# Kernel optimization log

Hardware: AMD Instinct MI355X
Metric: run time of the kernel (lower is better)

The kernel has to match this reference:

```python
import jax, jax.numpy as jnp
import numpy as np

NUM_HEADS = 16

def setup_inputs() -> dict:
    key = jax.random.key(0)
    ks = jax.random.split(key, 6)
    B, S, D = 2, 2048, 1024
    x = jax.random.normal(ks[0], (B, S, D), dtype=jnp.float32)
    s = 1.0 / np.sqrt(D)
    Wq = jax.random.normal(ks[1], (D, D), dtype=jnp.float32) * s
    Wk = jax.random.normal(ks[2], (D, D), dtype=jnp.float32) * s
    Wv = jax.random.normal(ks[3], (D, D), dtype=jnp.float32) * s
    Wff = jax.random.normal(ks[4], (D, D), dtype=jnp.float32) * s
    bff = jax.random.normal(ks[5], (D,), dtype=jnp.float32) * 0.01
    return {"x": x, "Wq": Wq, "Wk": Wk, "Wv": Wv, "Wff": Wff, "bff": bff}

def reference(x, Wq, Wk, Wv, Wff, bff):
    B, S, D = x.shape
    H = NUM_HEADS
    Dh = D // H
    # Q/K/V projections (bias-free Linears). Original scales Q by 1/sqrt(hidden_size).
    q = (x @ Wq.T) * (1.0 / jnp.sqrt(jnp.asarray(D, x.dtype)))
    k = x @ Wk.T
    v = x @ Wv.T
    q = q.reshape(B, S, H, Dh)
    k = k.reshape(B, S, H, Dh)
    v = v.reshape(B, S, H, Dh)
    # Blockwise online-softmax attention is mathematically identical to
    # full softmax attention over all keys (no causal mask in source).
    scores = jnp.einsum('bqhd,bkhd->bhqk', q, k)
    attn = jax.nn.softmax(scores, axis=-1)
    out = jnp.einsum('bhqk,bkhd->bqhd', attn, v).reshape(B, S, D)
    # Final feedforward Linear(hidden, hidden) with bias.
    return out @ Wff.T + bff
```

## Files before the change

kernel.cpp:

```cpp
#include <hip/hip_runtime.h>
#include <stdint.h>

typedef __attribute__((ext_vector_type(8))) short bf16x8;
typedef __attribute__((ext_vector_type(4))) float f32x4;

__device__ __forceinline__ uint16_t f2bf(float f) {
  union { float f; uint32_t u; } a; a.f = f;
  uint32_t u = a.u;
  u += 0x7FFFu + ((u >> 16) & 1u);
  return (uint16_t)(u >> 16);
}

__device__ __forceinline__ uint32_t pk_bf16(float a, float b) {
#if __has_builtin(__builtin_amdgcn_cvt_pk_bf16_f32)
  auto r = __builtin_amdgcn_cvt_pk_bf16_f32(a, b);
  uint32_t u; __builtin_memcpy(&u, &r, sizeof(u));
  return u;
#else
  return (uint32_t)f2bf(a) | ((uint32_t)f2bf(b) << 16);
#endif
}

__device__ __forceinline__ uint32_t pk_bf16_fast(float a, float b) {
#if __has_builtin(__builtin_amdgcn_cvt_pk_bf16_f32)
  auto r = __builtin_amdgcn_cvt_pk_bf16_f32(a, b);
  uint32_t u; __builtin_memcpy(&u, &r, sizeof(u));
  return u;
#else
  uint32_t ua, ub;
  __builtin_memcpy(&ua, &a, 4); __builtin_memcpy(&ub, &b, 4);
  return __builtin_amdgcn_perm(ub, ua, 0x07060302u);
#endif
}

__device__ __forceinline__ float fast_exp2(float x) {
#if __has_builtin(__builtin_amdgcn_exp2f)
  return __builtin_amdgcn_exp2f(x);
#else
  return exp2f(x);
#endif
}

__device__ __forceinline__ void gld_lds16(const uint16_t* g, uint16_t* l) {
  __builtin_amdgcn_global_load_lds(
      (const __attribute__((address_space(1))) void*)g,
      (__attribute__((address_space(3))) void*)l, 16, 0, 0);
}

__global__ void cast_all(const float* __restrict__ x, const float* __restrict__ wq,
                         const float* __restrict__ wk, const float* __restrict__ wv,
                         const float* __restrict__ wff,
                         uint16_t* __restrict__ xb, uint16_t* __restrict__ wqb,
                         uint16_t* __restrict__ wkb, uint16_t* __restrict__ wvb,
                         uint16_t* __restrict__ wffb) {
  int i = blockIdx.x * blockDim.x + threadIdx.x;
  const float* src; uint16_t* dst; int off;
  if (i < 1048576)      { src = x;   dst = xb;   off = i; }
  else if (i < 1310720) { src = wq;  dst = wqb;  off = i - 1048576; }
  else if (i < 1572864) { src = wk;  dst = wkb;  off = i - 1310720; }
  else if (i < 1835008) { src = wv;  dst = wvb;  off = i - 1572864; }
  else                  { src = wff; dst = wffb; off = i - 1835008; }
  float4 v = ((const float4*)src)[off];
  uint2 o; o.x = pk_bf16(v.x, v.y); o.y = pk_bf16(v.z, v.w);
  ((uint2*)dst)[off] = o;
}

__device__ __forceinline__ void gemm_tile(const uint16_t* __restrict__ Abase,
                                          const uint16_t* __restrict__ Bbase,
                                          uint16_t* lds, f32x4 acc[4][4]) {
  const int tid  = threadIdx.x;
  const int w    = tid >> 6;
  const int lane = tid & 63;
  const int wm   = w >> 1, wn = w & 1;
  const int lrow = lane & 15;
  const int quad = lane >> 4;
  const int srow = lane >> 3;
  const int lc   = (lane & 7) ^ srow;
  const int sx   = lrow & 7;
  uint16_t* a_lds = lds;
  uint16_t* b_lds = lds + 8192;

#pragma unroll
  for (int mt = 0; mt < 4; ++mt)
#pragma unroll
    for (int nt = 0; nt < 4; ++nt)
      acc[mt][nt] = (f32x4){0.f, 0.f, 0.f, 0.f};

  const uint16_t* ag = Abase + (size_t)(w * 32 + srow) * 1024 + lc * 8;
  const uint16_t* bg = Bbase + (size_t)(w * 32 + srow) * 1024 + lc * 8;

  for (int k0 = 0; k0 < 1024; k0 += 64) {
#pragma unroll
    for (int i8 = 0; i8 < 4; ++i8) {
      gld_lds16(ag + (size_t)i8 * 8 * 1024 + k0, a_lds + (w * 4 + i8) * 512);
      gld_lds16(bg + (size_t)i8 * 8 * 1024 + k0, b_lds + (w * 4 + i8) * 512);
    }
    __syncthreads();
#pragma unroll
    for (int ks = 0; ks < 2; ++ks) {
      bf16x8 af[4], bfr[4];
      const int c = ((ks * 4 + quad) ^ sx) << 3;
#pragma unroll
      for (int mt = 0; mt < 4; ++mt)
        af[mt] = *(const bf16x8*)(a_lds + (wm * 64 + mt * 16 + lrow) * 64 + c);
#pragma unroll
      for (int nt = 0; nt < 4; ++nt)
        bfr[nt] = *(const bf16x8*)(b_lds + (wn * 64 + nt * 16 + lrow) * 64 + c);
#pragma unroll
      for (int mt = 0; mt < 4; ++mt)
#pragma unroll
        for (int nt = 0; nt < 4; ++nt)
          acc[mt][nt] = __builtin_amdgcn_mfma_f32_16x16x32_bf16(af[mt], bfr[nt], acc[mt][nt], 0, 0, 0);
    }
    __syncthreads();
  }
}

__global__ __launch_bounds__(256) void gemm_qkv(
    const uint16_t* __restrict__ x,
    const uint16_t* __restrict__ wq, const uint16_t* __restrict__ wk, const uint16_t* __restrict__ wv,
    uint16_t* __restrict__ qo, uint16_t* __restrict__ ko, uint16_t* __restrict__ vto) {
  __shared__ __align__(16) uint16_t lds[17408];
  const int m0 = blockIdx.x * 128, n0 = blockIdx.y * 128, z = blockIdx.z;
  f32x4 acc[4][4];
  if (z < 2) {
    const uint16_t* W = (z == 0) ? wq : wk;
    gemm_tile(W + (size_t)n0 * 1024, x + (size_t)m0 * 1024, lds, acc);
  } else {
    gemm_tile(x + (size_t)m0 * 1024, wv + (size_t)n0 * 1024, lds, acc);
  }

  const int tid = threadIdx.x;
  const int lane = tid & 63, w = tid >> 6;
  const int wm = w >> 1, wn = w & 1, lrow = lane & 15, quad = lane >> 4;
  const float scale = (z == 0) ? 0.045084222f : 1.0f;

#pragma unroll
  for (int mt = 0; mt < 4; ++mt)
#pragma unroll
    for (int nt = 0; nt < 4; ++nt) {
      int i0 = wm * 64 + mt * 16 + quad * 4;
      int j  = wn * 64 + nt * 16 + lrow;
      uint2 dd;
      dd.x = pk_bf16(acc[mt][nt][0] * scale, acc[mt][nt][1] * scale);
      dd.y = pk_bf16(acc[mt][nt][2] * scale, acc[mt][nt][3] * scale);
      *(uint2*)(&lds[j * 136 + i0]) = dd;
    }
  __syncthreads();

  uint16_t* outp = (z == 0) ? qo : (z == 1) ? ko : vto;
  if (z < 2) {
#pragma unroll
    for (int it = 0; it < 8; ++it) {
      int idx = it * 256 + tid;
      int jj = idx >> 4, cc = idx & 15;
      uint4 v = *(const uint4*)(&lds[jj * 136 + cc * 8]);
      int m = m0 + jj, n = n0 + cc * 8;
      int b = m >> 11, s = m & 2047, h = n >> 6, dh = n & 63;
      *(uint4*)(outp + ((size_t)((b * 16 + h) * 2048 + s)) * 64 + dh) = v;
    }
  } else {
    int b = m0 >> 11, sbase = m0 & 2047;
#pragma unroll
    for (int it = 0; it < 8; ++it) {
      int idx = it * 256 + tid;
      int ff = idx >> 4, cc = idx & 15;
      uint4 v = *(const uint4*)(&lds[ff * 136 + cc * 8]);
      int n = n0 + ff, h = n >> 6, dh = n & 63;
      *(uint4*)(outp + ((size_t)((b * 16 + h) * 64 + dh)) * 2048 + sbase + cc * 8) = v;
    }
  }
}

__global__ __launch_bounds__(256) void gemm_ff(
    const uint16_t* __restrict__ ao, const uint16_t* __restrict__ wff,
    const float* __restrict__ bff, float* __restrict__ out) {
  __shared__ __align__(16) uint16_t lds[17408];
  const int m0 = blockIdx.x * 128, n0 = blockIdx.y * 128;
  f32x4 acc[4][4];
  gemm_tile(wff + (size_t)n0 * 1024, ao + (size_t)m0 * 1024, lds, acc);

  const int tid = threadIdx.x;
  const int lane = tid & 63, w = tid >> 6;
  const int wm = w >> 1, wn = w & 1, lrow = lane & 15, quad = lane >> 4;
  float* fl = (float*)lds;

#pragma unroll
  for (int p = 0; p < 2; ++p) {
    if (wm == p) {
#pragma unroll
      for (int mt = 0; mt < 4; ++mt)
#pragma unroll
        for (int nt = 0; nt < 4; ++nt) {
          int i0 = mt * 16 + quad * 4;
          int j  = wn * 64 + nt * 16 + lrow;
          *(f32x4*)(&fl[j * 68 + i0]) = acc[mt][nt];
        }
    }
    __syncthreads();
#pragma unroll
    for (int it = 0; it < 8; ++it) {
      int idx = it * 256 + tid;
      int jj = idx >> 4, cc = idx & 15;
      f32x4 v = *(const f32x4*)(&fl[jj * 68 + cc * 4]);
      int n = n0 + p * 64 + cc * 4;
      f32x4 bias = *(const f32x4*)(bff + n);
      f32x4 vv = v + bias;
      *(f32x4*)(out + (size_t)(m0 + jj) * 1024 + n) = vv;
    }
    __syncthreads();
  }
}

__global__ __launch_bounds__(256, 2) void attn(
    const uint16_t* __restrict__ q, const uint16_t* __restrict__ k,
    const uint16_t* __restrict__ vt, uint16_t* __restrict__ ao) {
  __shared__ __align__(16) uint16_t k_lds[2][4096];
  __shared__ __align__(16) uint16_t v_lds[2][4096];
  __shared__ __align__(16) uint16_t p_lds[4][2048];
  const int tid = threadIdx.x, w = tid >> 6, lane = tid & 63;
  const int lrow = lane & 15, quad = lane >> 4;
  const int srow = lane >> 3, lc = (lane & 7) ^ srow, sx = lrow & 7;
  const int bh = blockIdx.y, qb = blockIdx.x;
  const uint16_t* Q = q  + (size_t)bh * (2048 * 64);
  const uint16_t* K = k  + (size_t)bh * (2048 * 64);
  const uint16_t* V = vt + (size_t)bh * (64 * 2048);
  uint16_t* pw = p_lds[w];
  const int cswz = (lrow & 7) << 1;

  const int qr0 = qb * 128 + w * 32;
  bf16x8 qf[2][2];
#pragma unroll
  for (int qh = 0; qh < 2; ++qh)
#pragma unroll
    for (int ks = 0; ks < 2; ++ks)
      qf[qh][ks] = *(const bf16x8*)(Q + (size_t)(qr0 + qh * 16 + lrow) * 64 + ks * 32 + quad * 8);

  f32x4 o[2][4];
#pragma unroll
  for (int qh = 0; qh < 2; ++qh)
#pragma unroll
    for (int dt = 0; dt < 4; ++dt) o[qh][dt] = (f32x4){0.f, 0.f, 0.f, 0.f};
  float ls[2] = {0.f, 0.f};

  auto stage = [&](int kb, int bi) {
#pragma unroll
    for (int i2 = 0; i2 < 2; ++i2) {
      int i8 = w * 2 + i2;
      gld_lds16(K + (size_t)(kb * 64 + i8 * 8 + srow) * 64 + lc * 8, &k_lds[bi][i8 * 512]);
      gld_lds16(V + (size_t)(i8 * 8 + srow) * 2048 + kb * 64 + lc * 8, &v_lds[bi][i8 * 512]);
    }
  };
  stage(0, 0);

  for (int kb = 0; kb < 32; ++kb) {
    const int bi = kb & 1;
    __syncthreads();
    if (kb + 1 < 32) stage(kb + 1, bi ^ 1);

    f32x4 s[2][4];
#pragma unroll
    for (int qh = 0; qh < 2; ++qh)
#pragma unroll
      for (int kt = 0; kt < 4; ++kt) s[qh][kt] = (f32x4){0.f, 0.f, 0.f, 0.f};
#pragma unroll
    for (int ks = 0; ks < 2; ++ks) {
      const int c = ((ks * 4 + quad) ^ sx) << 3;
#pragma unroll
      for (int kt = 0; kt < 4; ++kt) {
        bf16x8 kf = *(const bf16x8*)(&k_lds[bi][(kt * 16 + lrow) * 64 + c]);
        s[0][kt] = __builtin_amdgcn_mfma_f32_16x16x32_bf16(kf, qf[0][ks], s[0][kt], 0, 0, 0);
        s[1][kt] = __builtin_amdgcn_mfma_f32_16x16x32_bf16(kf, qf[1][ks], s[1][kt], 0, 0, 0);
      }
    }

#pragma unroll
    for (int qh = 0; qh < 2; ++qh)
#pragma unroll
      for (int kt = 0; kt < 4; ++kt) {
        float p0 = fast_exp2(s[qh][kt][0]);
        float p1 = fast_exp2(s[qh][kt][1]);
        float p2 = fast_exp2(s[qh][kt][2]);
        float p3 = fast_exp2(s[qh][kt][3]);
        ls[qh] += (p0 + p1) + (p2 + p3);
        uint2 dd; dd.x = pk_bf16_fast(p0, p1); dd.y = pk_bf16_fast(p2, p3);
        *(uint2*)(pw + (qh * 16 + lrow) * 64 + (((kt * 4 + quad) ^ cswz) << 2)) = dd;
      }

#pragma unroll
    for (int ks = 0; ks < 2; ++ks) {
      bf16x8 pa0 = *(const bf16x8*)(pw + lrow * 64 + (((ks * 8 + quad * 2) ^ cswz) << 2));
      bf16x8 pa1 = *(const bf16x8*)(pw + (16 + lrow) * 64 + (((ks * 8 + quad * 2) ^ cswz) << 2));
      const int c = ((ks * 4 + quad) ^ sx) << 3;
#pragma unroll
      for (int dt = 0; dt < 4; ++dt) {
        bf16x8 vf = *(const bf16x8*)(&v_lds[bi][(dt * 16 + lrow) * 64 + c]);
        o[0][dt] = __builtin_amdgcn_mfma_f32_16x16x32_bf16(vf, pa0, o[0][dt], 0, 0, 0);
        o[1][dt] = __builtin_amdgcn_mfma_f32_16x16x32_bf16(vf, pa1, o[1][dt], 0, 0, 0);
      }
    }
  }

  const int b = bh >> 4, h = bh & 15;
#pragma unroll
  for (int qh = 0; qh < 2; ++qh) {
    float l = ls[qh];
    l += __shfl_xor(l, 16);
    l += __shfl_xor(l, 32);
    float inv = 1.0f / l;
    int sg = qr0 + qh * 16 + lrow;
#pragma unroll
    for (int dt = 0; dt < 4; ++dt) {
      uint2 dd;
      dd.x = pk_bf16(o[qh][dt][0] * inv, o[qh][dt][1] * inv);
      dd.y = pk_bf16(o[qh][dt][2] * inv, o[qh][dt][3] * inv);
      *(uint2*)(ao + (size_t)(b * 2048 + sg) * 1024 + h * 64 + dt * 16 + quad * 4) = dd;
    }
  }
}

extern "C" void kernel_launch(void* const* d_in, const int* in_sizes, int n_in,
                              void* d_out, int out_size, void* d_ws, size_t ws_size,
                              hipStream_t stream) {
  const float* x   = (const float*)d_in[0];
  const float* Wq  = (const float*)d_in[1];
  const float* Wk  = (const float*)d_in[2];
  const float* Wv  = (const float*)d_in[3];
  const float* Wff = (const float*)d_in[4];
  const float* bff = (const float*)d_in[5];
  float* out = (float*)d_out;

  uint16_t* ws = (uint16_t*)d_ws;
  uint16_t* x_bf   = ws;
  uint16_t* wq_bf  = ws + 4194304;
  uint16_t* wk_bf  = ws + 5242880;
  uint16_t* wv_bf  = ws + 6291456;
  uint16_t* wff_bf = ws + 7340032;
  uint16_t* q_bf   = ws + 8388608;
  uint16_t* k_bf   = ws + 12582912;
  uint16_t* vt_bf  = ws + 16777216;
  uint16_t* ao_bf  = ws + 20971520;

  cast_all<<<8192, 256, 0, stream>>>(x, Wq, Wk, Wv, Wff, x_bf, wq_bf, wk_bf, wv_bf, wff_bf);

  gemm_qkv<<<dim3(32, 8, 3), 256, 0, stream>>>(x_bf, wq_bf, wk_bf, wv_bf, q_bf, k_bf, vt_bf);
  attn<<<dim3(16, 32), 256, 0, stream>>>(q_bf, k_bf, vt_bf, ao_bf);
  gemm_ff<<<dim3(32, 8), 256, 0, stream>>>(ao_bf, wff_bf, bff, out);
}
```

Measured before the change: 190.8 us.

## Fuse Q and K projections to share x tile loads across two weight matrices

Splits the combined QKV GEMM into a Q+K kernel that loads each x tile once and multiplies it against both Wq and Wk tiles, accumulating two output tiles per block, plus a separate V kernel. The aim is to cut global and LDS traffic for x and halve the block count for Q/K. In exchange each thread holds twice the accumulators, which raises register pressure and may lower occupancy, and the extra kernel launch for V adds a small fixed overhead. The Q/K kernel also uses single-buffered loads with a larger LDS footprint.

```diff
diff --git a/kernel.cpp b/kernel.cpp
--- a/kernel.cpp
+++ b/kernel.cpp
@@ -116,40 +116,83 @@
   }
 }
 
-__global__ __launch_bounds__(256) void gemm_qkv(
+__global__ __launch_bounds__(256, 2) void gemm_qk(
     const uint16_t* __restrict__ x,
-    const uint16_t* __restrict__ wq, const uint16_t* __restrict__ wk, const uint16_t* __restrict__ wv,
-    uint16_t* __restrict__ qo, uint16_t* __restrict__ ko, uint16_t* __restrict__ vto) {
-  __shared__ __align__(16) uint16_t lds[17408];
-  const int m0 = blockIdx.x * 128, n0 = blockIdx.y * 128, z = blockIdx.z;
-  f32x4 acc[4][4];
-  if (z < 2) {
-    const uint16_t* W = (z == 0) ? wq : wk;
-    gemm_tile(W + (size_t)n0 * 1024, x + (size_t)m0 * 1024, lds, acc);
-  } else {
-    gemm_tile(x + (size_t)m0 * 1024, wv + (size_t)n0 * 1024, lds, acc);
-  }
-
-  const int tid = threadIdx.x;
-  const int lane = tid & 63, w = tid >> 6;
+    const uint16_t* __restrict__ wq, const uint16_t* __restrict__ wk,
+    uint16_t* __restrict__ qo, uint16_t* __restrict__ ko) {
+  __shared__ __align__(16) uint16_t lds[24576];
+  const int m0 = blockIdx.x * 128, n0 = blockIdx.y * 128;
+  const int tid = threadIdx.x, w = tid >> 6, lane = tid & 63;
   const int wm = w >> 1, wn = w & 1, lrow = lane & 15, quad = lane >> 4;
-  const float scale = (z == 0) ? 0.045084222f : 1.0f;
-
-#pragma unroll
-  for (int mt = 0; mt < 4; ++mt)
-#pragma unroll
-    for (int nt = 0; nt < 4; ++nt) {
-      int i0 = wm * 64 + mt * 16 + quad * 4;
-      int j  = wn * 64 + nt * 16 + lrow;
-      uint2 dd;
-      dd.x = pk_bf16(acc[mt][nt][0] * scale, acc[mt][nt][1] * scale);
-      dd.y = pk_bf16(acc[mt][nt][2] * scale, acc[mt][nt][3] * scale);
-      *(uint2*)(&lds[j * 136 + i0]) = dd;
-    }
-  __syncthreads();
-
-  uint16_t* outp = (z == 0) ? qo : (z == 1) ? ko : vto;
-  if (z < 2) {
+  const int srow = lane >> 3, lc = (lane & 7) ^ srow, sx = lrow & 7;
+  uint16_t* x_lds = lds;
+  uint16_t* wq_lds = lds + 8192;
+  uint16_t* wk_lds = lds + 16384;
+
+  f32x4 acc[2][4][4];
+#pragma unroll
+  for (int z = 0; z < 2; ++z)
+#pragma unroll
+    for (int mt = 0; mt < 4; ++mt)
+#pragma unroll
+      for (int nt = 0; nt < 4; ++nt)
+        acc[z][mt][nt] = (f32x4){0.f, 0.f, 0.f, 0.f};
+
+  const uint16_t* xg = x  + (size_t)(m0 + w * 32 + srow) * 1024 + lc * 8;
+  const uint16_t* qg = wq + (size_t)(n0 + w * 32 + srow) * 1024 + lc * 8;
+  const uint16_t* kg = wk + (size_t)(n0 + w * 32 + srow) * 1024 + lc * 8;
+
+  for (int k0 = 0; k0 < 1024; k0 += 64) {
+#pragma unroll
+    for (int i8 = 0; i8 < 4; ++i8) {
+      gld_lds16(xg + (size_t)i8 * 8 * 1024 + k0, x_lds  + (w * 4 + i8) * 512);
+      gld_lds16(qg + (size_t)i8 * 8 * 1024 + k0, wq_lds + (w * 4 + i8) * 512);
+      gld_lds16(kg + (size_t)i8 * 8 * 1024 + k0, wk_lds + (w * 4 + i8) * 512);
+    }
+    __syncthreads();
+#pragma unroll
+    for (int ks = 0; ks < 2; ++ks) {
+      const int c = ((ks * 4 + quad) ^ sx) << 3;
+      bf16x8 xb[4], wa[4];
+#pragma unroll
+      for (int nt = 0; nt < 4; ++nt)
+        xb[nt] = *(const bf16x8*)(x_lds + (wn * 64 + nt * 16 + lrow) * 64 + c);
+#pragma unroll
+      for (int mt = 0; mt < 4; ++mt)
+        wa[mt] = *(const bf16x8*)(wq_lds + (wm * 64 + mt * 16 + lrow) * 64 + c);
+#pragma unroll
+      for (int mt = 0; mt < 4; ++mt)
+#pragma unroll
+        for (int nt = 0; nt < 4; ++nt)
+          acc[0][mt][nt] = __builtin_amdgcn_mfma_f32_16x16x32_bf16(wa[mt], xb[nt], acc[0][mt][nt], 0, 0, 0);
+#pragma unroll
+      for (int mt = 0; mt < 4; ++mt)
+        wa[mt] = *(const bf16x8*)(wk_lds + (wm * 64 + mt * 16 + lrow) * 64 + c);
+#pragma unroll
+      for (int mt = 0; mt < 4; ++mt)
+#pragma unroll
+        for (int nt = 0; nt < 4; ++nt)
+          acc[1][mt][nt] = __builtin_amdgcn_mfma_f32_16x16x32_bf16(wa[mt], xb[nt], acc[1][mt][nt], 0, 0, 0);
+    }
+    __syncthreads();
+  }
+
+#pragma unroll
+  for (int z = 0; z < 2; ++z) {
+    const float scale = (z == 0) ? 0.045084222f : 1.0f;
+#pragma unroll
+    for (int mt = 0; mt < 4; ++mt)
+#pragma unroll
+      for (int nt = 0; nt < 4; ++nt) {
+        int i0 = wm * 64 + mt * 16 + quad * 4;
+        int j  = wn * 64 + nt * 16 + lrow;
+        uint2 dd;
+        dd.x = pk_bf16(acc[z][mt][nt][0] * scale, acc[z][mt][nt][1] * scale);
+        dd.y = pk_bf16(acc[z][mt][nt][2] * scale, acc[z][mt][nt][3] * scale);
+        *(uint2*)(&lds[j * 136 + i0]) = dd;
+      }
+    __syncthreads();
+    uint16_t* outp = (z == 0) ? qo : ko;
 #pragma unroll
     for (int it = 0; it < 8; ++it) {
       int idx = it * 256 + tid;
@@ -159,16 +202,43 @@
       int b = m >> 11, s = m & 2047, h = n >> 6, dh = n & 63;
       *(uint4*)(outp + ((size_t)((b * 16 + h) * 2048 + s)) * 64 + dh) = v;
     }
-  } else {
-    int b = m0 >> 11, sbase = m0 & 2047;
-#pragma unroll
-    for (int it = 0; it < 8; ++it) {
-      int idx = it * 256 + tid;
-      int ff = idx >> 4, cc = idx & 15;
-      uint4 v = *(const uint4*)(&lds[ff * 136 + cc * 8]);
-      int n = n0 + ff, h = n >> 6, dh = n & 63;
-      *(uint4*)(outp + ((size_t)((b * 16 + h) * 64 + dh)) * 2048 + sbase + cc * 8) = v;
-    }
+    __syncthreads();
+  }
+}
+
+__global__ __launch_bounds__(256) void gemm_v(
+    const uint16_t* __restrict__ x, const uint16_t* __restrict__ wv,
+    uint16_t* __restrict__ vto) {
+  __shared__ __align__(16) uint16_t lds[17408];
+  const int m0 = blockIdx.x * 128, n0 = blockIdx.y * 128;
+  f32x4 acc[4][4];
+  gemm_tile(x + (size_t)m0 * 1024, wv + (size_t)n0 * 1024, lds, acc);
+
+  const int tid = threadIdx.x;
+  const int lane = tid & 63, w = tid >> 6;
+  const int wm = w >> 1, wn = w & 1, lrow = lane & 15, quad = lane >> 4;
+
+#pragma unroll
+  for (int mt = 0; mt < 4; ++mt)
+#pragma unroll
+    for (int nt = 0; nt < 4; ++nt) {
+      int i0 = wm * 64 + mt * 16 + quad * 4;
+      int j  = wn * 64 + nt * 16 + lrow;
+      uint2 dd;
+      dd.x = pk_bf16(acc[mt][nt][0], acc[mt][nt][1]);
+      dd.y = pk_bf16(acc[mt][nt][2], acc[mt][nt][3]);
+      *(uint2*)(&lds[j * 136 + i0]) = dd;
+    }
+  __syncthreads();
+
+  int b = m0 >> 11, sbase = m0 & 2047;
+#pragma unroll
+  for (int it = 0; it < 8; ++it) {
+    int idx = it * 256 + tid;
+    int ff = idx >> 4, cc = idx & 15;
+    uint4 v = *(const uint4*)(&lds[ff * 136 + cc * 8]);
+    int n = n0 + ff, h = n >> 6, dh = n & 63;
+    *(uint4*)(vto + ((size_t)((b * 16 + h) * 64 + dh)) * 2048 + sbase + cc * 8) = v;
   }
 }
 
@@ -343,7 +413,8 @@
 
   cast_all<<<8192, 256, 0, stream>>>(x, Wq, Wk, Wv, Wff, x_bf, wq_bf, wk_bf, wv_bf, wff_bf);
 
-  gemm_qkv<<<dim3(32, 8, 3), 256, 0, stream>>>(x_bf, wq_bf, wk_bf, wv_bf, q_bf, k_bf, vt_bf);
+  gemm_qk<<<dim3(32, 8), 256, 0, stream>>>(x_bf, wq_bf, wk_bf, q_bf, k_bf);
+  gemm_v<<<dim3(32, 8), 256, 0, stream>>>(x_bf, wv_bf, vt_bf);
   attn<<<dim3(16, 32), 256, 0, stream>>>(q_bf, k_bf, vt_bf, ao_bf);
   gemm_ff<<<dim3(32, 8), 256, 0, stream>>>(ao_bf, wff_bf, bff, out);
 }
```

Result: slower. 203.2 us (+6.5%).
